# Kernel tuning notes

Hardware: AMD Instinct MI355X
Metric: run time of the kernel (lower is better)

Reference implementation:

```python
import jax, jax.numpy as jnp
import numpy as np

N = 50000        # nodes
E = 800000       # edges (avg degree 16)
D = 128          # input_dim
H = 128          # hidden_channels
OUT = 1          # output_dim
NUM_GRAPHS = 512 # graphs in batch (fixed for jit; == batch.max()+1)


def setup_inputs() -> dict:
    key = jax.random.key(0)
    ks = jax.random.split(key, 12)
    x = jax.random.normal(ks[0], (N, D), dtype=jnp.float32)
    edge_index = jax.random.randint(ks[1], (2, E), 0, N, dtype=jnp.int64)
    batch = jnp.sort(jax.random.randint(ks[2], (N,), 0, NUM_GRAPHS, dtype=jnp.int64))
    init = lambda k, shape, fan: jax.random.normal(k, shape, jnp.float32) * np.float32(1.0 / np.sqrt(fan))
    W1 = init(ks[3], (D, H), D); b1 = jnp.zeros((H,), jnp.float32)
    W2 = init(ks[4], (H, H), H); b2 = jnp.zeros((H,), jnp.float32)
    W3 = init(ks[5], (H, H), H); b3 = jnp.zeros((H,), jnp.float32)
    Wo = init(ks[6], (H, OUT), H); bo = jnp.zeros((OUT,), jnp.float32)
    return {"x": x, "edge_index": edge_index, "batch": batch,
            "W1": W1, "b1": b1, "W2": W2, "b2": b2, "W3": W3, "b3": b3,
            "Wo": Wo, "bo": bo}


def _gcn_layer(h, W, b, src, dst, dinv_sqrt):
    # GCNConv: x' = D^{-1/2}(A+I)D^{-1/2} X W + b  (self-loops added)
    hw = h @ W                                        # [N, H]
    coef = (dinv_sqrt[src] * dinv_sqrt[dst])[:, None] # [E, 1]
    agg = jax.ops.segment_sum(hw[src] * coef, dst, num_segments=N)
    agg = agg + hw * (dinv_sqrt * dinv_sqrt)[:, None] # self-loop term: deg^{-1}
    return agg + b


def reference(x, edge_index, batch, W1, b1, W2, b2, W3, b3, Wo, bo):
    src, dst = edge_index[0], edge_index[1]
    # degree from A+I (PyG computes deg on the target/col index)
    deg = jax.ops.segment_sum(jnp.ones((E,), x.dtype), dst, num_segments=N) + 1.0
    dinv_sqrt = jax.lax.rsqrt(deg)
    h = jax.nn.relu(_gcn_layer(x, W1, b1, src, dst, dinv_sqrt))
    h = jax.nn.relu(_gcn_layer(h, W2, b2, src, dst, dinv_sqrt))
    h = _gcn_layer(h, W3, b3, src, dst, dinv_sqrt)   # last conv: no relu
    pooled = jax.ops.segment_sum(h, batch, num_segments=NUM_GRAPHS)  # global_add_pool
    # F.dropout(p=0.1) is identity in eval mode
    return pooled @ Wo + bo                           # [NUM_GRAPHS, 1]
```

## Files before the change

### kernel.cpp

```cpp
#include <hip/hip_runtime.h>

typedef _Float16 f16;
typedef unsigned short u16;
typedef __attribute__((ext_vector_type(2))) _Float16 f16x2;
typedef __attribute__((ext_vector_type(8))) _Float16 f16x8;
typedef __attribute__((ext_vector_type(8))) unsigned short u16x8;
typedef __attribute__((ext_vector_type(4))) float f32x4;
typedef __attribute__((ext_vector_type(4))) int intx4;

#define STRIDE 64
#define SLAB   5120

__device__ inline float2 h2f(unsigned u){
    f16x2 h = __builtin_bit_cast(f16x2, u);
    return make_float2((float)h.x, (float)h.y);
}

__device__ inline void addrow(float* acc, uint4 u){
    float2 p0 = h2f(u.x), p1 = h2f(u.y), p2 = h2f(u.z), p3 = h2f(u.w);
    acc[0] += p0.x; acc[1] += p0.y; acc[2] += p1.x; acc[3] += p1.y;
    acc[4] += p2.x; acc[5] += p2.y; acc[6] += p3.x; acc[7] += p3.y;
}


__global__ __launch_bounds__(256) void k_bucket(const int* __restrict__ src, const int* __restrict__ dst,
                                                int* __restrict__ bucketCnt, unsigned* __restrict__ bucketBuf,
                                                int NB, int E4, int E){
    __shared__ int hist[256], pos[256];
    int t = threadIdx.x;
    hist[t] = 0;
    __syncthreads();
    int i4a = blockIdx.x*512 + t;
    int i4b = i4a + 256;
    bool va = i4a < E4, vb = i4b < E4;
    intx4 da = {}, db = {}, sa = {}, sb = {};
    if (va){ da = __builtin_nontemporal_load((const intx4*)dst + i4a);
             sa = __builtin_nontemporal_load((const intx4*)src + i4a); }
    if (vb){ db = __builtin_nontemporal_load((const intx4*)dst + i4b);
             sb = __builtin_nontemporal_load((const intx4*)src + i4b); }
    auto cnt1 = [&](int e, int d){ if (e < E) atomicAdd(&hist[d >> 8], 1); };
    if (va){ int b0 = i4a*4; cnt1(b0,da.x); cnt1(b0+1,da.y); cnt1(b0+2,da.z); cnt1(b0+3,da.w); }
    if (vb){ int b0 = i4b*4; cnt1(b0,db.x); cnt1(b0+1,db.y); cnt1(b0+2,db.z); cnt1(b0+3,db.w); }
    __syncthreads();
    if (t < NB && hist[t] > 0) pos[t] = atomicAdd(&bucketCnt[t], hist[t]);
    __syncthreads();
    auto put1 = [&](int e, int d, int s){
        if (e < E){
            int b = d >> 8;
            int slot = atomicAdd(&pos[b], 1);
            if (slot < SLAB)
                bucketBuf[(size_t)b*SLAB + slot] = ((unsigned)(d & 255) << 16) | (unsigned)s;
        }
    };
    if (va){ int b0 = i4a*4; put1(b0,da.x,sa.x); put1(b0+1,da.y,sa.y); put1(b0+2,da.z,sa.z); put1(b0+3,da.w,sa.w); }
    if (vb){ int b0 = i4b*4; put1(b0,db.x,sb.x); put1(b0+1,db.y,sb.y); put1(b0+2,db.z,sb.z); put1(b0+3,db.w,sb.w); }
}


__global__ __launch_bounds__(256) void k_build(const unsigned* __restrict__ bucketBuf,
                                               const int* __restrict__ bucketCnt,
                                               u16* __restrict__ csr, int* __restrict__ fil,
                                               float* __restrict__ dinv, int* __restrict__ blkh, int N){
    __shared__ u16 rows[256*64];
    __shared__ int cnt[256];
    __shared__ int h8[8];
    int t = threadIdx.x;
    cnt[t] = 0;
    if (t < 8) h8[t] = 0;
    u16x8 fillv;
    #pragma unroll
    for (int j = 0; j < 8; ++j) fillv[j] = (u16)N;
    #pragma unroll
    for (int j = 0; j < 8; ++j) *(u16x8*)&rows[t*64 + j*8] = fillv;
    __syncthreads();
    int b = blockIdx.x;
    int cb = min(bucketCnt[b], SLAB);
    for (int e = t; e < cb; e += 256){
        unsigned v = bucketBuf[(size_t)b*SLAB + e];
        int off = v >> 16;
        int p = atomicAdd(&cnt[off], 1);
        if (p < STRIDE){
            int ch = ((p >> 3) ^ (off & 7));
            rows[off*64 + ch*8 + (p & 7)] = (u16)(v & 0xffff);
        }
    }
    __syncthreads();
    int node = b*256 + t;
    if (node <= N){
        int c = cnt[t];
        fil[node] = c;
        dinv[node] = rsqrtf((float)c + 1.0f);
        if (node < N){
            int nb = (min(c, STRIDE) + 7) >> 3;
            if (nb > 7) nb = 7;
            atomicAdd(&h8[nb], 1);
        }
        u16x8* d8 = (u16x8*)&csr[(size_t)node*64];
        #pragma unroll
        for (int j = 0; j < 8; ++j)
            d8[j] = *(u16x8*)&rows[t*64 + ((j ^ (t & 7))*8)];
    }
    __syncthreads();
    if (t < 8) blkh[b*8 + t] = h8[t];
}

__global__ __launch_bounds__(256) void k_bscan(const int* __restrict__ blkh, int* __restrict__ blkoff,
                                               int* __restrict__ ord, uint4* __restrict__ hwrows,
                                               int N, int NQ4, int nbB){
    __shared__ int sm[8][256];
    int t = threadIdx.x;
    int v[8];
    #pragma unroll
    for (int b = 0; b < 8; ++b){
        v[b] = (t < nbB) ? blkh[t*8 + b] : 0;
        sm[b][t] = v[b];
    }
    __syncthreads();
    for (int off = 1; off < 256; off <<= 1){
        int u[8];
        #pragma unroll
        for (int b = 0; b < 8; ++b) u[b] = (t >= off) ? sm[b][t-off] : 0;
        __syncthreads();
        #pragma unroll
        for (int b = 0; b < 8; ++b) sm[b][t] += u[b];
        __syncthreads();
    }
    int s = 0;
    int bases[8];
    #pragma unroll
    for (int b = 0; b < 8; ++b){ bases[b] = s; s += sm[b][255]; }
    if (t < nbB){
        #pragma unroll
        for (int b = 0; b < 8; ++b)
            blkoff[t*8 + b] = sm[b][t] - v[b] + bases[b];
    }
    if (t >= 200 && t < 216) hwrows[(size_t)N*16 + (t - 200)] = make_uint4(0,0,0,0);
    for (int i = N + t; i < NQ4; i += 256) ord[i] = N;
}

__global__ __launch_bounds__(256) void k_scatterL(const int* __restrict__ fil, const int* __restrict__ blkoff,
                                                  int* __restrict__ ord, int N){
    __shared__ int off[8];
    int t = threadIdx.x;
    if (t < 8) off[t] = blkoff[blockIdx.x*8 + t];
    __syncthreads();
    int i = blockIdx.x*256 + t;
    if (i < N){
        int nb = (min(fil[i], STRIDE) + 7) >> 3;
        if (nb > 7) nb = 7;
        int p = atomicAdd(&off[nb], 1);
        ord[p] = i;
    }
}


__global__ __launch_bounds__(128) void k_prep(const float* __restrict__ W3, const float* __restrict__ Wo,
                                              const float* __restrict__ b3, float* __restrict__ u,
                                              float* __restrict__ su, float* __restrict__ zs,
                                              float* __restrict__ out, const float* __restrict__ bo,
                                              int N, int G){
    __shared__ float sWo[128];
    __shared__ float red[128];
    int t = threadIdx.x;
    sWo[t] = Wo[t];
    __syncthreads();
    float s = 0.f;
    for (int c2 = 0; c2 < 128; ++c2) s = fmaf(W3[t*128 + c2], sWo[c2], s);
    u[t] = s;
    red[t] = b3[t] * sWo[t];
    __syncthreads();
    for (int o = 64; o > 0; o >>= 1){
        if (t < o) red[t] += red[t+o];
        __syncthreads();
    }
    if (t == 0){ *su = red[0]; zs[N] = 0.f; }
    float bv = bo[0];
    for (int g2 = t; g2 < G; g2 += 128) out[g2] = bv;
}


#define LDW 136

template<int AFP16>
__global__ __launch_bounds__(256) void k_mm(const void* __restrict__ Av, const float* __restrict__ W,
                                            const float* __restrict__ dinv, f16* __restrict__ C, int n){
    __shared__ __align__(16) _Float16 sWt[128*LDW];
    __shared__ __align__(16) _Float16 sOut[4][16*LDW];
    int t = threadIdx.x;
    for (int idx = t; idx < 4096; idx += 256){
        int k = idx >> 5, c4 = (idx & 31) * 4;
        float4 w = ((const float4*)W)[idx];
        sWt[(c4+0)*LDW + k] = (f16)w.x;
        sWt[(c4+1)*LDW + k] = (f16)w.y;
        sWt[(c4+2)*LDW + k] = (f16)w.z;
        sWt[(c4+3)*LDW + k] = (f16)w.w;
    }
    __syncthreads();

    int wv = t >> 6, l = t & 63;
    int r16 = l & 15, g = l >> 4;
    int r0 = blockIdx.x * 64 + wv * 16;

    int arow = r0 + r16;
    bool aok = arow < n;
    f16x8 a[4];
    #pragma unroll
    for (int s = 0; s < 4; ++s){
        if (AFP16){
            const f16* A = (const f16*)Av;
            a[s] = aok ? *(const f16x8*)&A[(size_t)arow*128 + s*32 + g*8] : (f16x8)(_Float16)0.f;
        } else {
            const float* A = (const float*)Av;
            f16x8 av = (f16x8)(_Float16)0.f;
            if (aok){
                const float4* ap = (const float4*)&A[(size_t)arow*128 + s*32 + g*8];
                float4 x0 = ap[0], x1 = ap[1];
                av[0]=(f16)x0.x; av[1]=(f16)x0.y; av[2]=(f16)x0.z; av[3]=(f16)x0.w;
                av[4]=(f16)x1.x; av[5]=(f16)x1.y; av[6]=(f16)x1.z; av[7]=(f16)x1.w;
            }
            a[s] = av;
        }
    }

    f32x4 acc[8];
    #pragma unroll
    for (int ct = 0; ct < 8; ++ct) acc[ct] = (f32x4)0.f;

    #pragma unroll
    for (int ct = 0; ct < 8; ++ct){
        int c = ct*16 + r16;
        #pragma unroll
        for (int s = 0; s < 4; ++s){
            f16x8 b = *(const f16x8*)&sWt[c*LDW + s*32 + g*8];
            acc[ct] = __builtin_amdgcn_mfma_f32_16x16x32_f16(a[s], b, acc[ct], 0, 0, 0);
        }
    }

    float dv[4];
    #pragma unroll
    for (int j = 0; j < 4; ++j){
        int rr = r0 + g*4 + j;
        dv[j] = (rr < n) ? dinv[rr] : 0.f;
    }
    #pragma unroll
    for (int ct = 0; ct < 8; ++ct)
        #pragma unroll
        for (int j = 0; j < 4; ++j)
            sOut[wv][(g*4+j)*LDW + ct*16 + r16] = (f16)(acc[ct][j] * dv[j]);
    __syncthreads();

    int orow = r0 + r16;
    if (orow < n){
        const f16x8* srcp = (const f16x8*)&sOut[wv][r16*LDW + g*32];
        f16x8 o0 = srcp[0], o1 = srcp[1], o2 = srcp[2], o3 = srcp[3];
        f16x8* dstp = (f16x8*)&C[(size_t)orow*128 + g*32];
        dstp[0]=o0; dstp[1]=o1; dstp[2]=o2; dstp[3]=o3;
    }
}


#define AGG_BODY \
    int l = threadIdx.x & 63; \
    int g = l >> 4, c = l & 15; \
    intx4 wq = *((const intx4*)ord + wvi); \
    int w0 = __builtin_amdgcn_readfirstlane(wq.x); \
    int w1 = __builtin_amdgcn_readfirstlane(wq.y); \
    int w2 = __builtin_amdgcn_readfirstlane(wq.z); \
    int w3 = __builtin_amdgcn_readfirstlane(wq.w); \
    int wsel = (g==0) ? w0 : (g==1) ? w1 : (g==2) ? w2 : w3; \
    const uint4* rows = (const uint4*)hw; \
    float acc[8] = {0,0,0,0,0,0,0,0}; \
    { uint4 s = rows[(size_t)wsel*16 + c]; addrow(acc, s); } \
    int nb0=(min(fil[w0],STRIDE)+7)>>3, nb1=(min(fil[w1],STRIDE)+7)>>3; \
    int nb2=(min(fil[w2],STRIDE)+7)>>3, nb3=(min(fil[w3],STRIDE)+7)>>3; \
    int nbm  = max(max(nb0,nb1), max(nb2,nb3)); \
    int nbsel = (g==0) ? nb0 : (g==1) ? nb1 : (g==2) ? nb2 : nb3; \
    const u16* cp = csr + (size_t)wsel*STRIDE; \
    for (int t2 = 0; t2 < nbm; ++t2){ \
        if (t2 < nbsel){ \
            u16x8 iv = *(const u16x8*)cp; cp += 8; \
            uint4 r0 = rows[(size_t)iv[0]*16 + c]; \
            uint4 r1 = rows[(size_t)iv[1]*16 + c]; \
            uint4 r2 = rows[(size_t)iv[2]*16 + c]; \
            uint4 r3 = rows[(size_t)iv[3]*16 + c]; \
            uint4 r4 = rows[(size_t)iv[4]*16 + c]; \
            uint4 r5 = rows[(size_t)iv[5]*16 + c]; \
            uint4 r6 = rows[(size_t)iv[6]*16 + c]; \
            uint4 r7 = rows[(size_t)iv[7]*16 + c]; \
            addrow(acc, r0); addrow(acc, r1); addrow(acc, r2); addrow(acc, r3); \
            addrow(acc, r4); addrow(acc, r5); addrow(acc, r6); addrow(acc, r7); \
        } \
    }

__global__ __launch_bounds__(256) void k_agg4(const f16* __restrict__ hw, const float* __restrict__ dinv,
                                              const int* __restrict__ fil, const u16* __restrict__ csr,
                                              const int* __restrict__ ord, const float* __restrict__ bias,
                                              f16* __restrict__ hout, int N, int NQ){
    int wvi = (blockIdx.x*256 + threadIdx.x) >> 6;
    if (wvi >= NQ) return;
    AGG_BODY
    if (wsel < N){
        float di = dinv[wsel];
        const float4* bp = (const float4*)bias + c*2;
        float4 b0 = bp[0], b1 = bp[1];
        f16x8 o;
        o[0]=(f16)fmaxf(fmaf(acc[0],di,b0.x),0.f); o[1]=(f16)fmaxf(fmaf(acc[1],di,b0.y),0.f);
        o[2]=(f16)fmaxf(fmaf(acc[2],di,b0.z),0.f); o[3]=(f16)fmaxf(fmaf(acc[3],di,b0.w),0.f);
        o[4]=(f16)fmaxf(fmaf(acc[4],di,b1.x),0.f); o[5]=(f16)fmaxf(fmaf(acc[5],di,b1.y),0.f);
        o[6]=(f16)fmaxf(fmaf(acc[6],di,b1.z),0.f); o[7]=(f16)fmaxf(fmaf(acc[7],di,b1.w),0.f);
        *(f16x8*)&hout[(size_t)wsel*128 + c*8] = o;
    }
}

__global__ __launch_bounds__(256) void k_agg4z(const f16* __restrict__ hw, const float* __restrict__ dinv,
                                               const int* __restrict__ fil, const u16* __restrict__ csr,
                                               const int* __restrict__ ord, const float* __restrict__ bias,
                                               const float* __restrict__ u, float* __restrict__ zs,
                                               int N, int NQ){
    int wvi = (blockIdx.x*256 + threadIdx.x) >> 6;
    if (wvi >= NQ) return;
    AGG_BODY
    float di = dinv[wsel];
    const float4* bp = (const float4*)bias + c*2;
    const float4* up = (const float4*)u    + c*2;
    float4 b0 = bp[0], b1 = bp[1];
    float4 u0 = up[0], u1 = up[1];
    float dot = fmaxf(fmaf(acc[0],di,b0.x),0.f)*u0.x + fmaxf(fmaf(acc[1],di,b0.y),0.f)*u0.y
              + fmaxf(fmaf(acc[2],di,b0.z),0.f)*u0.z + fmaxf(fmaf(acc[3],di,b0.w),0.f)*u0.w
              + fmaxf(fmaf(acc[4],di,b1.x),0.f)*u1.x + fmaxf(fmaf(acc[5],di,b1.y),0.f)*u1.y
              + fmaxf(fmaf(acc[6],di,b1.z),0.f)*u1.z + fmaxf(fmaf(acc[7],di,b1.w),0.f)*u1.w;
    dot += __shfl_xor(dot, 1);
    dot += __shfl_xor(dot, 2);
    dot += __shfl_xor(dot, 4);
    dot += __shfl_xor(dot, 8);
    if (c == 0 && wsel < N) zs[wsel] = di * dot;
}


__global__ __launch_bounds__(256) void k_aggs(const float* __restrict__ zs, const float* __restrict__ dinv,
                                              const int* __restrict__ fil, const u16* __restrict__ csr,
                                              const int* __restrict__ batch, const float* __restrict__ supt,
                                              float* __restrict__ out, int N){
    __shared__ float bins[512];
    int t = threadIdx.x;
    bins[t] = 0.f; bins[t+256] = 0.f;
    __syncthreads();
    int i = blockIdx.x*256 + t;
    if (i < N){
        float acc = zs[i];
        int nb = (min(fil[i], STRIDE) + 7) >> 3;
        const u16* cp = csr + (size_t)i*STRIDE;
        for (int b = 0; b < nb; ++b){
            u16x8 iv = *(const u16x8*)cp; cp += 8;
            float s0 = zs[iv[0]] + zs[iv[1]], s1 = zs[iv[2]] + zs[iv[3]];
            float s2 = zs[iv[4]] + zs[iv[5]], s3 = zs[iv[6]] + zs[iv[7]];
            acc += (s0 + s1) + (s2 + s3);
        }
        float tv = fmaf(dinv[i], acc, *supt);
        atomicAdd(&bins[batch[i]], tv);
    }
    __syncthreads();
    float v0 = bins[t], v1 = bins[t+256];
    if (v0 != 0.f) atomicAdd(&out[t], v0);
    if (v1 != 0.f) atomicAdd(&out[t+256], v1);
}


extern "C" void kernel_launch(void* const* d_in, const int* in_sizes, int n_in,
                              void* d_out, int out_size, void* d_ws, size_t ws_size,
                              hipStream_t stream) {
    const float* x     = (const float*)d_in[0];
    const int*   ei    = (const int*)d_in[1];
    const int*   batch = (const int*)d_in[2];
    const float* W1 = (const float*)d_in[3];
    const float* b1 = (const float*)d_in[4];
    const float* W2 = (const float*)d_in[5];
    const float* b2 = (const float*)d_in[6];
    const float* W3 = (const float*)d_in[7];
    const float* b3 = (const float*)d_in[8];
    const float* Wo = (const float*)d_in[9];
    const float* bo = (const float*)d_in[10];

    int N = in_sizes[0] / 128;
    int E = in_sizes[1] / 2;
    int G = out_size;
    const int* srcI = ei;
    const int* dstI = ei + E;

    int NQ  = (N + 3) / 4;
    int NQ4 = NQ * 4;
    int NB  = (N + 256) / 256;
    int E4  = (E + 3) / 4;
    int nbK = (E + 2047) / 2048;

    char* p = (char*)d_ws;
    size_t off = 0;
    auto alloc = [&](size_t bytes) -> void* {
        void* r = p + off;
        off += (bytes + 255) & ~(size_t)255;
        return r;
    };
    f16*      hw      = (f16*)alloc((size_t)(N+1)*128*sizeof(f16));
    f16*      h       = (f16*)alloc((size_t)N*128*sizeof(f16));
    float*    dinv    = (float*)alloc((size_t)(N+1)*sizeof(float));
    int*      fil     = (int*)alloc((size_t)(N+1)*sizeof(int));
    int*      blkh    = (int*)alloc((size_t)NB*8*sizeof(int));
    int*      blkoff  = (int*)alloc((size_t)NB*8*sizeof(int));
    int*      ord     = (int*)alloc((size_t)NQ4*sizeof(int));
    float*    zs      = (float*)alloc((size_t)(N+1)*sizeof(float));
    float*    uvec    = (float*)alloc(128*sizeof(float));
    float*    su      = (float*)alloc(sizeof(float));
    int*      bucketCnt = (int*)alloc((size_t)NB*sizeof(int));
    unsigned* bucketBuf = (unsigned*)alloc((size_t)NB*SLAB*sizeof(unsigned));
    u16*      csr     = (u16*)alloc((size_t)(N+1)*STRIDE*sizeof(u16));

    hipMemsetAsync(bucketCnt, 0, (size_t)NB*sizeof(int), stream);

    k_bucket  <<<nbK, 256, 0, stream>>>(srcI, dstI, bucketCnt, bucketBuf, NB, E4, E);
    k_build   <<<NB,  256, 0, stream>>>(bucketBuf, bucketCnt, csr, fil, dinv, blkh, N);
    k_bscan   <<<1,   256, 0, stream>>>(blkh, blkoff, ord, (uint4*)hw, N, NQ4, NB);
    k_scatterL<<<NB,  256, 0, stream>>>(fil, blkoff, ord, N);
    k_prep    <<<1,   128, 0, stream>>>(W3, Wo, b3, uvec, su, zs, (float*)d_out, bo, N, G);

    int nbM = (N + 63)/64;
    int nbA = (int)(((size_t)NQ*64 + 255)/256);

    k_mm<0> <<<nbM, 256, 0, stream>>>(x, W1, dinv, hw, N);
    k_agg4  <<<nbA, 256, 0, stream>>>(hw, dinv, fil, csr, ord, b1, h, N, NQ);
    k_mm<1> <<<nbM, 256, 0, stream>>>(h, W2, dinv, hw, N);
    k_agg4z <<<nbA, 256, 0, stream>>>(hw, dinv, fil, csr, ord, b2, uvec, zs, N, NQ);
    k_aggs  <<<NB,  256, 0, stream>>>(zs, dinv, fil, csr, batch, su, (float*)d_out, N);
}
```

Before: 161.6 us.

## Fuse all GCN pipeline stages into one cooperative persistent kernel with grid syncs

Replaces the chain of ten kernel launches plus a memset with a single cooperative persistent kernel. Each former kernel becomes a grid-stride phase separated by grid.sync(), and a shared-memory union is reused across phases. The aim is to remove launch gaps and the tails of the small single-block kernels. In exchange it pays for grid-wide barriers, the matmul phase now serialises its four waves' output staging through one smaller sOut buffer, and host occupancy queries run on every call. The old multi-kernel path stays as a fallback.

```diff
diff --git a/kernel.cpp b/kernel.cpp
--- a/kernel.cpp
+++ b/kernel.cpp
@@ -1,4 +1,7 @@
 #include <hip/hip_runtime.h>
+#include <hip/hip_cooperative_groups.h>
+
+namespace cg = cooperative_groups;
 
 typedef _Float16 f16;
 typedef unsigned short u16;
@@ -10,6 +13,7 @@
 
 #define STRIDE 64
 #define SLAB   5120
+#define LDW    136
 
 __device__ inline float2 h2f(unsigned u){
     f16x2 h = __builtin_bit_cast(f16x2, u);
@@ -21,243 +25,6 @@
     acc[0] += p0.x; acc[1] += p0.y; acc[2] += p1.x; acc[3] += p1.y;
     acc[4] += p2.x; acc[5] += p2.y; acc[6] += p3.x; acc[7] += p3.y;
 }
-
-
-__global__ __launch_bounds__(256) void k_bucket(const int* __restrict__ src, const int* __restrict__ dst,
-                                                int* __restrict__ bucketCnt, unsigned* __restrict__ bucketBuf,
-                                                int NB, int E4, int E){
-    __shared__ int hist[256], pos[256];
-    int t = threadIdx.x;
-    hist[t] = 0;
-    __syncthreads();
-    int i4a = blockIdx.x*512 + t;
-    int i4b = i4a + 256;
-    bool va = i4a < E4, vb = i4b < E4;
-    intx4 da = {}, db = {}, sa = {}, sb = {};
-    if (va){ da = __builtin_nontemporal_load((const intx4*)dst + i4a);
-             sa = __builtin_nontemporal_load((const intx4*)src + i4a); }
-    if (vb){ db = __builtin_nontemporal_load((const intx4*)dst + i4b);
-             sb = __builtin_nontemporal_load((const intx4*)src + i4b); }
-    auto cnt1 = [&](int e, int d){ if (e < E) atomicAdd(&hist[d >> 8], 1); };
-    if (va){ int b0 = i4a*4; cnt1(b0,da.x); cnt1(b0+1,da.y); cnt1(b0+2,da.z); cnt1(b0+3,da.w); }
-    if (vb){ int b0 = i4b*4; cnt1(b0,db.x); cnt1(b0+1,db.y); cnt1(b0+2,db.z); cnt1(b0+3,db.w); }
-    __syncthreads();
-    if (t < NB && hist[t] > 0) pos[t] = atomicAdd(&bucketCnt[t], hist[t]);
-    __syncthreads();
-    auto put1 = [&](int e, int d, int s){
-        if (e < E){
-            int b = d >> 8;
-            int slot = atomicAdd(&pos[b], 1);
-            if (slot < SLAB)
-                bucketBuf[(size_t)b*SLAB + slot] = ((unsigned)(d & 255) << 16) | (unsigned)s;
-        }
-    };
-    if (va){ int b0 = i4a*4; put1(b0,da.x,sa.x); put1(b0+1,da.y,sa.y); put1(b0+2,da.z,sa.z); put1(b0+3,da.w,sa.w); }
-    if (vb){ int b0 = i4b*4; put1(b0,db.x,sb.x); put1(b0+1,db.y,sb.y); put1(b0+2,db.z,sb.z); put1(b0+3,db.w,sb.w); }
-}
-
-
-__global__ __launch_bounds__(256) void k_build(const unsigned* __restrict__ bucketBuf,
-                                               const int* __restrict__ bucketCnt,
-                                               u16* __restrict__ csr, int* __restrict__ fil,
-                                               float* __restrict__ dinv, int* __restrict__ blkh, int N){
-    __shared__ u16 rows[256*64];
-    __shared__ int cnt[256];
-    __shared__ int h8[8];
-    int t = threadIdx.x;
-    cnt[t] = 0;
-    if (t < 8) h8[t] = 0;
-    u16x8 fillv;
-    #pragma unroll
-    for (int j = 0; j < 8; ++j) fillv[j] = (u16)N;
-    #pragma unroll
-    for (int j = 0; j < 8; ++j) *(u16x8*)&rows[t*64 + j*8] = fillv;
-    __syncthreads();
-    int b = blockIdx.x;
-    int cb = min(bucketCnt[b], SLAB);
-    for (int e = t; e < cb; e += 256){
-        unsigned v = bucketBuf[(size_t)b*SLAB + e];
-        int off = v >> 16;
-        int p = atomicAdd(&cnt[off], 1);
-        if (p < STRIDE){
-            int ch = ((p >> 3) ^ (off & 7));
-            rows[off*64 + ch*8 + (p & 7)] = (u16)(v & 0xffff);
-        }
-    }
-    __syncthreads();
-    int node = b*256 + t;
-    if (node <= N){
-        int c = cnt[t];
-        fil[node] = c;
-        dinv[node] = rsqrtf((float)c + 1.0f);
-        if (node < N){
-            int nb = (min(c, STRIDE) + 7) >> 3;
-            if (nb > 7) nb = 7;
-            atomicAdd(&h8[nb], 1);
-        }
-        u16x8* d8 = (u16x8*)&csr[(size_t)node*64];
-        #pragma unroll
-        for (int j = 0; j < 8; ++j)
-            d8[j] = *(u16x8*)&rows[t*64 + ((j ^ (t & 7))*8)];
-    }
-    __syncthreads();
-    if (t < 8) blkh[b*8 + t] = h8[t];
-}
-
-__global__ __launch_bounds__(256) void k_bscan(const int* __restrict__ blkh, int* __restrict__ blkoff,
-                                               int* __restrict__ ord, uint4* __restrict__ hwrows,
-                                               int N, int NQ4, int nbB){
-    __shared__ int sm[8][256];
-    int t = threadIdx.x;
-    int v[8];
-    #pragma unroll
-    for (int b = 0; b < 8; ++b){
-        v[b] = (t < nbB) ? blkh[t*8 + b] : 0;
-        sm[b][t] = v[b];
-    }
-    __syncthreads();
-    for (int off = 1; off < 256; off <<= 1){
-        int u[8];
-        #pragma unroll
-        for (int b = 0; b < 8; ++b) u[b] = (t >= off) ? sm[b][t-off] : 0;
-        __syncthreads();
-        #pragma unroll
-        for (int b = 0; b < 8; ++b) sm[b][t] += u[b];
-        __syncthreads();
-    }
-    int s = 0;
-    int bases[8];
-    #pragma unroll
-    for (int b = 0; b < 8; ++b){ bases[b] = s; s += sm[b][255]; }
-    if (t < nbB){
-        #pragma unroll
-        for (int b = 0; b < 8; ++b)
-            blkoff[t*8 + b] = sm[b][t] - v[b] + bases[b];
-    }
-    if (t >= 200 && t < 216) hwrows[(size_t)N*16 + (t - 200)] = make_uint4(0,0,0,0);
-    for (int i = N + t; i < NQ4; i += 256) ord[i] = N;
-}
-
-__global__ __launch_bounds__(256) void k_scatterL(const int* __restrict__ fil, const int* __restrict__ blkoff,
-                                                  int* __restrict__ ord, int N){
-    __shared__ int off[8];
-    int t = threadIdx.x;
-    if (t < 8) off[t] = blkoff[blockIdx.x*8 + t];
-    __syncthreads();
-    int i = blockIdx.x*256 + t;
-    if (i < N){
-        int nb = (min(fil[i], STRIDE) + 7) >> 3;
-        if (nb > 7) nb = 7;
-        int p = atomicAdd(&off[nb], 1);
-        ord[p] = i;
-    }
-}
-
-
-__global__ __launch_bounds__(128) void k_prep(const float* __restrict__ W3, const float* __restrict__ Wo,
-                                              const float* __restrict__ b3, float* __restrict__ u,
-                                              float* __restrict__ su, float* __restrict__ zs,
-                                              float* __restrict__ out, const float* __restrict__ bo,
-                                              int N, int G){
-    __shared__ float sWo[128];
-    __shared__ float red[128];
-    int t = threadIdx.x;
-    sWo[t] = Wo[t];
-    __syncthreads();
-    float s = 0.f;
-    for (int c2 = 0; c2 < 128; ++c2) s = fmaf(W3[t*128 + c2], sWo[c2], s);
-    u[t] = s;
-    red[t] = b3[t] * sWo[t];
-    __syncthreads();
-    for (int o = 64; o > 0; o >>= 1){
-        if (t < o) red[t] += red[t+o];
-        __syncthreads();
-    }
-    if (t == 0){ *su = red[0]; zs[N] = 0.f; }
-    float bv = bo[0];
-    for (int g2 = t; g2 < G; g2 += 128) out[g2] = bv;
-}
-
-
-#define LDW 136
-
-template<int AFP16>
-__global__ __launch_bounds__(256) void k_mm(const void* __restrict__ Av, const float* __restrict__ W,
-                                            const float* __restrict__ dinv, f16* __restrict__ C, int n){
-    __shared__ __align__(16) _Float16 sWt[128*LDW];
-    __shared__ __align__(16) _Float16 sOut[4][16*LDW];
-    int t = threadIdx.x;
-    for (int idx = t; idx < 4096; idx += 256){
-        int k = idx >> 5, c4 = (idx & 31) * 4;
-        float4 w = ((const float4*)W)[idx];
-        sWt[(c4+0)*LDW + k] = (f16)w.x;
-        sWt[(c4+1)*LDW + k] = (f16)w.y;
-        sWt[(c4+2)*LDW + k] = (f16)w.z;
-        sWt[(c4+3)*LDW + k] = (f16)w.w;
-    }
-    __syncthreads();
-
-    int wv = t >> 6, l = t & 63;
-    int r16 = l & 15, g = l >> 4;
-    int r0 = blockIdx.x * 64 + wv * 16;
-
-    int arow = r0 + r16;
-    bool aok = arow < n;
-    f16x8 a[4];
-    #pragma unroll
-    for (int s = 0; s < 4; ++s){
-        if (AFP16){
-            const f16* A = (const f16*)Av;
-            a[s] = aok ? *(const f16x8*)&A[(size_t)arow*128 + s*32 + g*8] : (f16x8)(_Float16)0.f;
-        } else {
-            const float* A = (const float*)Av;
-            f16x8 av = (f16x8)(_Float16)0.f;
-            if (aok){
-                const float4* ap = (const float4*)&A[(size_t)arow*128 + s*32 + g*8];
-                float4 x0 = ap[0], x1 = ap[1];
-                av[0]=(f16)x0.x; av[1]=(f16)x0.y; av[2]=(f16)x0.z; av[3]=(f16)x0.w;
-                av[4]=(f16)x1.x; av[5]=(f16)x1.y; av[6]=(f16)x1.z; av[7]=(f16)x1.w;
-            }
-            a[s] = av;
-        }
-    }
-
-    f32x4 acc[8];
-    #pragma unroll
-    for (int ct = 0; ct < 8; ++ct) acc[ct] = (f32x4)0.f;
-
-    #pragma unroll
-    for (int ct = 0; ct < 8; ++ct){
-        int c = ct*16 + r16;
-        #pragma unroll
-        for (int s = 0; s < 4; ++s){
-            f16x8 b = *(const f16x8*)&sWt[c*LDW + s*32 + g*8];
-            acc[ct] = __builtin_amdgcn_mfma_f32_16x16x32_f16(a[s], b, acc[ct], 0, 0, 0);
-        }
-    }
-
-    float dv[4];
-    #pragma unroll
-    for (int j = 0; j < 4; ++j){
-        int rr = r0 + g*4 + j;
-        dv[j] = (rr < n) ? dinv[rr] : 0.f;
-    }
-    #pragma unroll
-    for (int ct = 0; ct < 8; ++ct)
-        #pragma unroll
-        for (int j = 0; j < 4; ++j)
-            sOut[wv][(g*4+j)*LDW + ct*16 + r16] = (f16)(acc[ct][j] * dv[j]);
-    __syncthreads();
-
-    int orow = r0 + r16;
-    if (orow < n){
-        const f16x8* srcp = (const f16x8*)&sOut[wv][r16*LDW + g*32];
-        f16x8 o0 = srcp[0], o1 = srcp[1], o2 = srcp[2], o3 = srcp[3];
-        f16x8* dstp = (f16x8*)&C[(size_t)orow*128 + g*32];
-        dstp[0]=o0; dstp[1]=o1; dstp[2]=o2; dstp[3]=o3;
-    }
-}
-
 
 #define AGG_BODY \
     int l = threadIdx.x & 63; \
@@ -292,6 +59,496 @@
         } \
     }
 
+
+template<int AFP16>
+__device__ __forceinline__ void mm_body(const void* Av, const float* W, const float* dinv,
+                                        f16* C, int n, int vb, _Float16* sWt, _Float16* sOut){
+    int t = threadIdx.x;
+    for (int idx = t; idx < 4096; idx += 256){
+        int k = idx >> 5, c4 = (idx & 31) * 4;
+        float4 w = ((const float4*)W)[idx];
+        sWt[(c4+0)*LDW + k] = (f16)w.x;
+        sWt[(c4+1)*LDW + k] = (f16)w.y;
+        sWt[(c4+2)*LDW + k] = (f16)w.z;
+        sWt[(c4+3)*LDW + k] = (f16)w.w;
+    }
+    __syncthreads();
+
+    int wv = t >> 6, l = t & 63;
+    int r16 = l & 15, g = l >> 4;
+    int r0 = vb * 64 + wv * 16;
+
+    int arow = r0 + r16;
+    bool aok = arow < n;
+    f16x8 a[4];
+    #pragma unroll
+    for (int s = 0; s < 4; ++s){
+        if (AFP16){
+            const f16* A = (const f16*)Av;
+            a[s] = aok ? *(const f16x8*)&A[(size_t)arow*128 + s*32 + g*8] : (f16x8)(_Float16)0.f;
+        } else {
+            const float* A = (const float*)Av;
+            f16x8 av = (f16x8)(_Float16)0.f;
+            if (aok){
+                const float4* ap = (const float4*)&A[(size_t)arow*128 + s*32 + g*8];
+                float4 x0 = ap[0], x1 = ap[1];
+                av[0]=(f16)x0.x; av[1]=(f16)x0.y; av[2]=(f16)x0.z; av[3]=(f16)x0.w;
+                av[4]=(f16)x1.x; av[5]=(f16)x1.y; av[6]=(f16)x1.z; av[7]=(f16)x1.w;
+            }
+            a[s] = av;
+        }
+    }
+
+    f32x4 acc[8];
+    #pragma unroll
+    for (int ct = 0; ct < 8; ++ct) acc[ct] = (f32x4)0.f;
+    #pragma unroll
+    for (int ct = 0; ct < 8; ++ct){
+        int c = ct*16 + r16;
+        #pragma unroll
+        for (int s = 0; s < 4; ++s){
+            f16x8 b = *(const f16x8*)&sWt[c*LDW + s*32 + g*8];
+            acc[ct] = __builtin_amdgcn_mfma_f32_16x16x32_f16(a[s], b, acc[ct], 0, 0, 0);
+        }
+    }
+
+    float dv[4];
+    #pragma unroll
+    for (int j = 0; j < 4; ++j){
+        int rr = r0 + g*4 + j;
+        dv[j] = (rr < n) ? dinv[rr] : 0.f;
+    }
+    for (int s4 = 0; s4 < 4; ++s4){
+        if (wv == s4){
+            #pragma unroll
+            for (int ct = 0; ct < 8; ++ct)
+                #pragma unroll
+                for (int j = 0; j < 4; ++j)
+                    sOut[(g*4+j)*LDW + ct*16 + r16] = (f16)(acc[ct][j] * dv[j]);
+        }
+        __syncthreads();
+        if (wv == s4){
+            int orow = r0 + r16;
+            if (orow < n){
+                const f16x8* sp = (const f16x8*)&sOut[r16*LDW + g*32];
+                f16x8 o0 = sp[0], o1 = sp[1], o2 = sp[2], o3 = sp[3];
+                f16x8* dp = (f16x8*)&C[(size_t)orow*128 + g*32];
+                dp[0]=o0; dp[1]=o1; dp[2]=o2; dp[3]=o3;
+            }
+        }
+        __syncthreads();
+    }
+}
+
+
+struct Params {
+    const float* x; const int* srcI; const int* dstI; const int* batch;
+    const float* W1; const float* b1; const float* W2; const float* b2;
+    const float* W3; const float* b3; const float* Wo; const float* bo;
+    float* out;
+    f16* hw; f16* h; float* dinv; int* fil; int* blkh; int* blkoff;
+    int* ord; float* zs; float* uvec; float* su; int* bucketCnt; unsigned* bucketBuf;
+    u16* csr;
+    int N, E, E4, G, NB, NQ, NQ4, nbK, nbM;
+};
+
+__global__ __launch_bounds__(256, 4) void k_mega(Params P){
+    cg::grid_group grid = cg::this_grid();
+    int t = threadIdx.x;
+    int nP = gridDim.x;
+
+    __shared__ __align__(16) union {
+        struct { int hist[256]; int pos[256]; } bk;
+        struct { u16 rows[256*64]; int cnt[256]; int h8[8]; } bd;
+        struct { int sm[8][256]; } sc;
+        struct { _Float16 sWt[128*LDW]; _Float16 sOut[16*LDW]; } mm;
+        struct { float bins[512]; } ag;
+        struct { float sWo[128]; float red[128]; } pr;
+        struct { int off[8]; } st;
+    } S;
+
+    if (blockIdx.x == 0){
+        if (t < 128) S.pr.sWo[t] = P.Wo[t];
+        __syncthreads();
+        if (t < 128){
+            float s = 0.f;
+            for (int k = 0; k < 128; ++k) s = fmaf(P.W3[t*128 + k], S.pr.sWo[k], s);
+            P.uvec[t] = s;
+            S.pr.red[t] = P.b3[t] * S.pr.sWo[t];
+        }
+        __syncthreads();
+        for (int o = 64; o > 0; o >>= 1){
+            if (t < o && t < 128) S.pr.red[t] += S.pr.red[t+o];
+            __syncthreads();
+        }
+        if (t == 0){ *P.su = S.pr.red[0]; P.zs[P.N] = 0.f; }
+        float bv = P.bo[0];
+        for (int g2 = t; g2 < P.G; g2 += 256) P.out[g2] = bv;
+    } else {
+        for (int i = (blockIdx.x-1)*256 + t; i < P.NB; i += (nP-1)*256) P.bucketCnt[i] = 0;
+    }
+    grid.sync();
+
+    for (int vb = blockIdx.x; vb < P.nbK; vb += nP){
+        S.bk.hist[t] = 0;
+        __syncthreads();
+        int i4a = vb*512 + t, i4b = i4a + 256;
+        bool va = i4a < P.E4, vvb = i4b < P.E4;
+        intx4 da = {}, db = {}, sa = {}, sb = {};
+        if (va){ da = __builtin_nontemporal_load((const intx4*)P.dstI + i4a);
+                 sa = __builtin_nontemporal_load((const intx4*)P.srcI + i4a); }
+        if (vvb){ db = __builtin_nontemporal_load((const intx4*)P.dstI + i4b);
+                  sb = __builtin_nontemporal_load((const intx4*)P.srcI + i4b); }
+        auto cnt1 = [&](int e, int d){ if (e < P.E) atomicAdd(&S.bk.hist[d >> 8], 1); };
+        if (va){ int b0 = i4a*4; cnt1(b0,da.x); cnt1(b0+1,da.y); cnt1(b0+2,da.z); cnt1(b0+3,da.w); }
+        if (vvb){ int b0 = i4b*4; cnt1(b0,db.x); cnt1(b0+1,db.y); cnt1(b0+2,db.z); cnt1(b0+3,db.w); }
+        __syncthreads();
+        if (t < P.NB && S.bk.hist[t] > 0) S.bk.pos[t] = atomicAdd(&P.bucketCnt[t], S.bk.hist[t]);
+        __syncthreads();
+        auto put1 = [&](int e, int d, int s){
+            if (e < P.E){
+                int b = d >> 8;
+                int slot = atomicAdd(&S.bk.pos[b], 1);
+                if (slot < SLAB)
+                    P.bucketBuf[(size_t)b*SLAB + slot] = ((unsigned)(d & 255) << 16) | (unsigned)s;
+            }
+        };
+        if (va){ int b0 = i4a*4; put1(b0,da.x,sa.x); put1(b0+1,da.y,sa.y); put1(b0+2,da.z,sa.z); put1(b0+3,da.w,sa.w); }
+        if (vvb){ int b0 = i4b*4; put1(b0,db.x,sb.x); put1(b0+1,db.y,sb.y); put1(b0+2,db.z,sb.z); put1(b0+3,db.w,sb.w); }
+        __syncthreads();
+    }
+    grid.sync();
+
+    for (int vb = blockIdx.x; vb < P.NB; vb += nP){
+        S.bd.cnt[t] = 0;
+        if (t < 8) S.bd.h8[t] = 0;
+        u16x8 fillv;
+        #pragma unroll
+        for (int j = 0; j < 8; ++j) fillv[j] = (u16)P.N;
+        #pragma unroll
+        for (int j = 0; j < 8; ++j) *(u16x8*)&S.bd.rows[t*64 + j*8] = fillv;
+        __syncthreads();
+        int cb = min(P.bucketCnt[vb], SLAB);
+        for (int e = t; e < cb; e += 256){
+            unsigned v = P.bucketBuf[(size_t)vb*SLAB + e];
+            int off = v >> 16;
+            int slot = atomicAdd(&S.bd.cnt[off], 1);
+            if (slot < STRIDE){
+                int ch = ((slot >> 3) ^ (off & 7));
+                S.bd.rows[off*64 + ch*8 + (slot & 7)] = (u16)(v & 0xffff);
+            }
+        }
+        __syncthreads();
+        int node = vb*256 + t;
+        if (node <= P.N){
+            int c = S.bd.cnt[t];
+            P.fil[node] = c;
+            P.dinv[node] = rsqrtf((float)c + 1.0f);
+            if (node < P.N){
+                int nb = (min(c, STRIDE) + 7) >> 3;
+                if (nb > 7) nb = 7;
+                atomicAdd(&S.bd.h8[nb], 1);
+            }
+            u16x8* d8 = (u16x8*)&P.csr[(size_t)node*64];
+            #pragma unroll
+            for (int j = 0; j < 8; ++j)
+                d8[j] = *(u16x8*)&S.bd.rows[t*64 + ((j ^ (t & 7))*8)];
+        }
+        __syncthreads();
+        if (t < 8) P.blkh[vb*8 + t] = S.bd.h8[t];
+        __syncthreads();
+    }
+    grid.sync();
+
+    if (blockIdx.x == 0){
+        int v[8];
+        #pragma unroll
+        for (int b = 0; b < 8; ++b){
+            v[b] = (t < P.NB) ? P.blkh[t*8 + b] : 0;
+            S.sc.sm[b][t] = v[b];
+        }
+        __syncthreads();
+        for (int off = 1; off < 256; off <<= 1){
+            int u[8];
+            #pragma unroll
+            for (int b = 0; b < 8; ++b) u[b] = (t >= off) ? S.sc.sm[b][t-off] : 0;
+            __syncthreads();
+            #pragma unroll
+            for (int b = 0; b < 8; ++b) S.sc.sm[b][t] += u[b];
+            __syncthreads();
+        }
+        int s = 0;
+        int bases[8];
+        #pragma unroll
+        for (int b = 0; b < 8; ++b){ bases[b] = s; s += S.sc.sm[b][255]; }
+        if (t < P.NB){
+            #pragma unroll
+            for (int b = 0; b < 8; ++b)
+                P.blkoff[t*8 + b] = S.sc.sm[b][t] - v[b] + bases[b];
+        }
+    }
+    if (blockIdx.x == 1){
+        if (t < 16) ((uint4*)P.hw)[(size_t)P.N*16 + t] = make_uint4(0,0,0,0);
+        for (int i = P.N + t; i < P.NQ4; i += 256) P.ord[i] = P.N;
+    }
+    grid.sync();
+
+    for (int vb = blockIdx.x; vb < P.NB + P.nbM; vb += nP){
+        if (vb < P.NB){
+            if (t < 8) S.st.off[t] = P.blkoff[vb*8 + t];
+            __syncthreads();
+            int i = vb*256 + t;
+            if (i < P.N){
+                int nb = (min(P.fil[i], STRIDE) + 7) >> 3;
+                if (nb > 7) nb = 7;
+                int pos = atomicAdd(&S.st.off[nb], 1);
+                P.ord[pos] = i;
+            }
+            __syncthreads();
+        } else {
+            mm_body<0>(P.x, P.W1, P.dinv, P.hw, P.N, vb - P.NB, S.mm.sWt, S.mm.sOut);
+        }
+    }
+    grid.sync();
+
+    {
+        const f16* hw = P.hw; const int* fil = P.fil; const u16* csr = P.csr;
+        const int* ord = P.ord; int N = P.N;
+        int waveId = blockIdx.x*4 + (t >> 6);
+        int nW = nP*4;
+        for (int wvi = waveId; wvi < P.NQ; wvi += nW){
+            AGG_BODY
+            if (wsel < N){
+                float di = P.dinv[wsel];
+                const float4* bp = (const float4*)P.b1 + c*2;
+                float4 b0 = bp[0], b1v = bp[1];
+                f16x8 o;
+                o[0]=(f16)fmaxf(fmaf(acc[0],di,b0.x),0.f); o[1]=(f16)fmaxf(fmaf(acc[1],di,b0.y),0.f);
+                o[2]=(f16)fmaxf(fmaf(acc[2],di,b0.z),0.f); o[3]=(f16)fmaxf(fmaf(acc[3],di,b0.w),0.f);
+                o[4]=(f16)fmaxf(fmaf(acc[4],di,b1v.x),0.f); o[5]=(f16)fmaxf(fmaf(acc[5],di,b1v.y),0.f);
+                o[6]=(f16)fmaxf(fmaf(acc[6],di,b1v.z),0.f); o[7]=(f16)fmaxf(fmaf(acc[7],di,b1v.w),0.f);
+                *(f16x8*)&P.h[(size_t)wsel*128 + c*8] = o;
+            }
+        }
+    }
+    grid.sync();
+
+    for (int vb = blockIdx.x; vb < P.nbM; vb += nP)
+        mm_body<1>(P.h, P.W2, P.dinv, P.hw, P.N, vb, S.mm.sWt, S.mm.sOut);
+    grid.sync();
+
+    {
+        const f16* hw = P.hw; const int* fil = P.fil; const u16* csr = P.csr;
+        const int* ord = P.ord; int N = P.N;
+        int waveId = blockIdx.x*4 + (t >> 6);
+        int nW = nP*4;
+        for (int wvi = waveId; wvi < P.NQ; wvi += nW){
+            AGG_BODY
+            float di = P.dinv[wsel];
+            const float4* bp = (const float4*)P.b2 + c*2;
+            const float4* up = (const float4*)P.uvec + c*2;
+            float4 b0 = bp[0], b1v = bp[1];
+            float4 u0 = up[0], u1 = up[1];
+            float dot = fmaxf(fmaf(acc[0],di,b0.x),0.f)*u0.x + fmaxf(fmaf(acc[1],di,b0.y),0.f)*u0.y
+                      + fmaxf(fmaf(acc[2],di,b0.z),0.f)*u0.z + fmaxf(fmaf(acc[3],di,b0.w),0.f)*u0.w
+                      + fmaxf(fmaf(acc[4],di,b1v.x),0.f)*u1.x + fmaxf(fmaf(acc[5],di,b1v.y),0.f)*u1.y
+                      + fmaxf(fmaf(acc[6],di,b1v.z),0.f)*u1.z + fmaxf(fmaf(acc[7],di,b1v.w),0.f)*u1.w;
+            dot += __shfl_xor(dot, 1);
+            dot += __shfl_xor(dot, 2);
+            dot += __shfl_xor(dot, 4);
+            dot += __shfl_xor(dot, 8);
+            if (c == 0 && wsel < N) P.zs[wsel] = di * dot;
+        }
+    }
+    grid.sync();
+
+    for (int vb = blockIdx.x; vb < P.NB; vb += nP){
+        S.ag.bins[t] = 0.f; S.ag.bins[t+256] = 0.f;
+        __syncthreads();
+        int i = vb*256 + t;
+        if (i < P.N){
+            float acc = P.zs[i];
+            int nb = (min(P.fil[i], STRIDE) + 7) >> 3;
+            const u16* cp = P.csr + (size_t)i*STRIDE;
+            for (int b = 0; b < nb; ++b){
+                u16x8 iv = *(const u16x8*)cp; cp += 8;
+                float s0 = P.zs[iv[0]] + P.zs[iv[1]], s1 = P.zs[iv[2]] + P.zs[iv[3]];
+                float s2 = P.zs[iv[4]] + P.zs[iv[5]], s3 = P.zs[iv[6]] + P.zs[iv[7]];
+                acc += (s0 + s1) + (s2 + s3);
+            }
+            float tv = fmaf(P.dinv[i], acc, *P.su);
+            atomicAdd(&S.ag.bins[P.batch[i]], tv);
+        }
+        __syncthreads();
+        float v0 = S.ag.bins[t], v1 = S.ag.bins[t+256];
+        if (v0 != 0.f) atomicAdd(&P.out[t], v0);
+        if (v1 != 0.f) atomicAdd(&P.out[t+256], v1);
+        __syncthreads();
+    }
+}
+
+
+__global__ __launch_bounds__(256) void k_bucket(const int* __restrict__ src, const int* __restrict__ dst,
+                                                int* __restrict__ bucketCnt, unsigned* __restrict__ bucketBuf,
+                                                int NB, int E4, int E){
+    __shared__ int hist[256], pos[256];
+    int t = threadIdx.x;
+    hist[t] = 0;
+    __syncthreads();
+    int i4a = blockIdx.x*512 + t;
+    int i4b = i4a + 256;
+    bool va = i4a < E4, vb = i4b < E4;
+    intx4 da = {}, db = {}, sa = {}, sb = {};
+    if (va){ da = __builtin_nontemporal_load((const intx4*)dst + i4a);
+             sa = __builtin_nontemporal_load((const intx4*)src + i4a); }
+    if (vb){ db = __builtin_nontemporal_load((const intx4*)dst + i4b);
+             sb = __builtin_nontemporal_load((const intx4*)src + i4b); }
+    auto cnt1 = [&](int e, int d){ if (e < E) atomicAdd(&hist[d >> 8], 1); };
+    if (va){ int b0 = i4a*4; cnt1(b0,da.x); cnt1(b0+1,da.y); cnt1(b0+2,da.z); cnt1(b0+3,da.w); }
+    if (vb){ int b0 = i4b*4; cnt1(b0,db.x); cnt1(b0+1,db.y); cnt1(b0+2,db.z); cnt1(b0+3,db.w); }
+    __syncthreads();
+    if (t < NB && hist[t] > 0) pos[t] = atomicAdd(&bucketCnt[t], hist[t]);
+    __syncthreads();
+    auto put1 = [&](int e, int d, int s){
+        if (e < E){
+            int b = d >> 8;
+            int slot = atomicAdd(&pos[b], 1);
+            if (slot < SLAB)
+                bucketBuf[(size_t)b*SLAB + slot] = ((unsigned)(d & 255) << 16) | (unsigned)s;
+        }
+    };
+    if (va){ int b0 = i4a*4; put1(b0,da.x,sa.x); put1(b0+1,da.y,sa.y); put1(b0+2,da.z,sa.z); put1(b0+3,da.w,sa.w); }
+    if (vb){ int b0 = i4b*4; put1(b0,db.x,sb.x); put1(b0+1,db.y,sb.y); put1(b0+2,db.z,sb.z); put1(b0+3,db.w,sb.w); }
+}
+
+__global__ __launch_bounds__(256) void k_build(const unsigned* __restrict__ bucketBuf,
+                                               const int* __restrict__ bucketCnt,
+                                               u16* __restrict__ csr, int* __restrict__ fil,
+                                               float* __restrict__ dinv, int* __restrict__ blkh, int N){
+    __shared__ u16 rows[256*64];
+    __shared__ int cnt[256];
+    __shared__ int h8[8];
+    int t = threadIdx.x;
+    cnt[t] = 0;
+    if (t < 8) h8[t] = 0;
+    u16x8 fillv;
+    #pragma unroll
+    for (int j = 0; j < 8; ++j) fillv[j] = (u16)N;
+    #pragma unroll
+    for (int j = 0; j < 8; ++j) *(u16x8*)&rows[t*64 + j*8] = fillv;
+    __syncthreads();
+    int b = blockIdx.x;
+    int cb = min(bucketCnt[b], SLAB);
+    for (int e = t; e < cb; e += 256){
+        unsigned v = bucketBuf[(size_t)b*SLAB + e];
+        int off = v >> 16;
+        int p = atomicAdd(&cnt[off], 1);
+        if (p < STRIDE){
+            int ch = ((p >> 3) ^ (off & 7));
+            rows[off*64 + ch*8 + (p & 7)] = (u16)(v & 0xffff);
+        }
+    }
+    __syncthreads();
+    int node = b*256 + t;
+    if (node <= N){
+        int c = cnt[t];
+        fil[node] = c;
+        dinv[node] = rsqrtf((float)c + 1.0f);
+        if (node < N){
+            int nb = (min(c, STRIDE) + 7) >> 3;
+            if (nb > 7) nb = 7;
+            atomicAdd(&h8[nb], 1);
+        }
+        u16x8* d8 = (u16x8*)&csr[(size_t)node*64];
+        #pragma unroll
+        for (int j = 0; j < 8; ++j)
+            d8[j] = *(u16x8*)&rows[t*64 + ((j ^ (t & 7))*8)];
+    }
+    __syncthreads();
+    if (t < 8) blkh[b*8 + t] = h8[t];
+}
+
+__global__ __launch_bounds__(256) void k_bscan(const int* __restrict__ blkh, int* __restrict__ blkoff,
+                                               int* __restrict__ ord, uint4* __restrict__ hwrows,
+                                               int N, int NQ4, int nbB){
+    __shared__ int sm[8][256];
+    int t = threadIdx.x;
+    int v[8];
+    #pragma unroll
+    for (int b = 0; b < 8; ++b){
+        v[b] = (t < nbB) ? blkh[t*8 + b] : 0;
+        sm[b][t] = v[b];
+    }
+    __syncthreads();
+    for (int off = 1; off < 256; off <<= 1){
+        int u[8];
+        #pragma unroll
+        for (int b = 0; b < 8; ++b) u[b] = (t >= off) ? sm[b][t-off] : 0;
+        __syncthreads();
+        #pragma unroll
+        for (int b = 0; b < 8; ++b) sm[b][t] += u[b];
+        __syncthreads();
+    }
+    int s = 0;
+    int bases[8];
+    #pragma unroll
+    for (int b = 0; b < 8; ++b){ bases[b] = s; s += sm[b][255]; }
+    if (t < nbB){
+        #pragma unroll
+        for (int b = 0; b < 8; ++b)
+            blkoff[t*8 + b] = sm[b][t] - v[b] + bases[b];
+    }
+    if (t >= 200 && t < 216) hwrows[(size_t)N*16 + (t - 200)] = make_uint4(0,0,0,0);
+    for (int i = N + t; i < NQ4; i += 256) ord[i] = N;
+}
+
+__global__ __launch_bounds__(256) void k_scatterL(const int* __restrict__ fil, const int* __restrict__ blkoff,
+                                                  int* __restrict__ ord, int N){
+    __shared__ int off[8];
+    int t = threadIdx.x;
+    if (t < 8) off[t] = blkoff[blockIdx.x*8 + t];
+    __syncthreads();
+    int i = blockIdx.x*256 + t;
+    if (i < N){
+        int nb = (min(fil[i], STRIDE) + 7) >> 3;
+        if (nb > 7) nb = 7;
+        int p = atomicAdd(&off[nb], 1);
+        ord[p] = i;
+    }
+}
+
+__global__ __launch_bounds__(128) void k_prep(const float* __restrict__ W3, const float* __restrict__ Wo,
+                                              const float* __restrict__ b3, float* __restrict__ u,
+                                              float* __restrict__ su, float* __restrict__ zs,
+                                              float* __restrict__ out, const float* __restrict__ bo,
+                                              int N, int G){
+    __shared__ float sWo[128];
+    __shared__ float red[128];
+    int t = threadIdx.x;
+    sWo[t] = Wo[t];
+    __syncthreads();
+    float s = 0.f;
+    for (int c2 = 0; c2 < 128; ++c2) s = fmaf(W3[t*128 + c2], sWo[c2], s);
+    u[t] = s;
+    red[t] = b3[t] * sWo[t];
+    __syncthreads();
+    for (int o = 64; o > 0; o >>= 1){
+        if (t < o) red[t] += red[t+o];
+        __syncthreads();
+    }
+    if (t == 0){ *su = red[0]; zs[N] = 0.f; }
+    float bv = bo[0];
+    for (int g2 = t; g2 < G; g2 += 128) out[g2] = bv;
+}
+
+template<int AFP16>
+__global__ __launch_bounds__(256) void k_mm(const void* __restrict__ Av, const float* __restrict__ W,
+                                            const float* __restrict__ dinv, f16* __restrict__ C, int n){
+    __shared__ __align__(16) _Float16 sWt[128*LDW];
+    __shared__ __align__(16) _Float16 sOut[16*LDW];
+    mm_body<AFP16>(Av, W, dinv, C, n, blockIdx.x, sWt, sOut);
+}
+
 __global__ __launch_bounds__(256) void k_agg4(const f16* __restrict__ hw, const float* __restrict__ dinv,
                                               const int* __restrict__ fil, const u16* __restrict__ csr,
                                               const int* __restrict__ ord, const float* __restrict__ bias,
@@ -336,7 +593,6 @@
     if (c == 0 && wsel < N) zs[wsel] = di * dot;
 }
 
-
 __global__ __launch_bounds__(256) void k_aggs(const float* __restrict__ zs, const float* __restrict__ dinv,
                                               const int* __restrict__ fil, const u16* __restrict__ csr,
                                               const int* __restrict__ batch, const float* __restrict__ supt,
@@ -392,6 +648,7 @@
     int NB  = (N + 256) / 256;
     int E4  = (E + 3) / 4;
     int nbK = (E + 2047) / 2048;
+    int nbM = (N + 63) / 64;
 
     char* p = (char*)d_ws;
     size_t off = 0;
@@ -409,25 +666,50 @@
     int*      ord     = (int*)alloc((size_t)NQ4*sizeof(int));
     float*    zs      = (float*)alloc((size_t)(N+1)*sizeof(float));
     float*    uvec    = (float*)alloc(128*sizeof(float));
-    float*    su      = (float*)alloc(sizeof(float));
+    float*    su      = (float*)alloc(256);
     int*      bucketCnt = (int*)alloc((size_t)NB*sizeof(int));
     unsigned* bucketBuf = (unsigned*)alloc((size_t)NB*SLAB*sizeof(unsigned));
     u16*      csr     = (u16*)alloc((size_t)(N+1)*STRIDE*sizeof(u16));
 
-    hipMemsetAsync(bucketCnt, 0, (size_t)NB*sizeof(int), stream);
-
-    k_bucket  <<<nbK, 256, 0, stream>>>(srcI, dstI, bucketCnt, bucketBuf, NB, E4, E);
-    k_build   <<<NB,  256, 0, stream>>>(bucketBuf, bucketCnt, csr, fil, dinv, blkh, N);
-    k_bscan   <<<1,   256, 0, stream>>>(blkh, blkoff, ord, (uint4*)hw, N, NQ4, NB);
-    k_scatterL<<<NB,  256, 0, stream>>>(fil, blkoff, ord, N);
-    k_prep    <<<1,   128, 0, stream>>>(W3, Wo, b3, uvec, su, zs, (float*)d_out, bo, N, G);
-
-    int nbM = (N + 63)/64;
-    int nbA = (int)(((size_t)NQ*64 + 255)/256);
-
-    k_mm<0> <<<nbM, 256, 0, stream>>>(x, W1, dinv, hw, N);
-    k_agg4  <<<nbA, 256, 0, stream>>>(hw, dinv, fil, csr, ord, b1, h, N, NQ);
-    k_mm<1> <<<nbM, 256, 0, stream>>>(h, W2, dinv, hw, N);
-    k_agg4z <<<nbA, 256, 0, stream>>>(hw, dinv, fil, csr, ord, b2, uvec, zs, N, NQ);
-    k_aggs  <<<NB,  256, 0, stream>>>(zs, dinv, fil, csr, batch, su, (float*)d_out, N);
-}
+    int coop = 0, dev = 0, nCU = 0, blkPerCU = 0;
+    hipGetDevice(&dev);
+    hipDeviceGetAttribute(&coop, hipDeviceAttributeCooperativeLaunch, dev);
+    hipDeviceGetAttribute(&nCU, hipDeviceAttributeMultiprocessorCount, dev);
+    hipError_t occ = hipOccupancyMaxActiveBlocksPerMultiprocessor(&blkPerCU, k_mega, 256, 0);
+
+    bool done = false;
+    if (coop && occ == hipSuccess && blkPerCU > 0 && nCU > 0){
+        Params prm;
+        prm.x = x; prm.srcI = srcI; prm.dstI = dstI; prm.batch = batch;
+        prm.W1 = W1; prm.b1 = b1; prm.W2 = W2; prm.b2 = b2;
+        prm.W3 = W3; prm.b3 = b3; prm.Wo = Wo; prm.bo = bo;
+        prm.out = (float*)d_out;
+        prm.hw = hw; prm.h = h; prm.dinv = dinv; prm.fil = fil;
+        prm.blkh = blkh; prm.blkoff = blkoff; prm.ord = ord; prm.zs = zs;
+        prm.uvec = uvec; prm.su = su; prm.bucketCnt = bucketCnt; prm.bucketBuf = bucketBuf;
+        prm.csr = csr;
+        prm.N = N; prm.E = E; prm.E4 = E4; prm.G = G; prm.NB = NB;
+        prm.NQ = NQ; prm.NQ4 = NQ4; prm.nbK = nbK; prm.nbM = nbM;
+
+        int grid = blkPerCU * nCU;
+        if (grid > 2048) grid = 2048;
+        void* args[] = { (void*)&prm };
+        hipError_t err = hipLaunchCooperativeKernel(k_mega, dim3(grid), dim3(256), args, 0u, stream);
+        if (err == hipSuccess) done = true;
+    }
+
+    if (!done){
+        hipMemsetAsync(bucketCnt, 0, (size_t)NB*sizeof(int), stream);
+        k_bucket  <<<nbK, 256, 0, stream>>>(srcI, dstI, bucketCnt, bucketBuf, NB, E4, E);
+        k_build   <<<NB,  256, 0, stream>>>(bucketBuf, bucketCnt, csr, fil, dinv, blkh, N);
+        k_bscan   <<<1,   256, 0, stream>>>(blkh, blkoff, ord, (uint4*)hw, N, NQ4, NB);
+        k_scatterL<<<NB,  256, 0, stream>>>(fil, blkoff, ord, N);
+        k_prep    <<<1,   128, 0, stream>>>(W3, Wo, b3, uvec, su, zs, (float*)d_out, bo, N, G);
+        int nbA = (int)(((size_t)NQ*64 + 255)/256);
+        k_mm<0> <<<nbM, 256, 0, stream>>>(x, W1, dinv, hw, N);
+        k_agg4  <<<nbA, 256, 0, stream>>>(hw, dinv, fil, csr, ord, b1, h, N, NQ);
+        k_mm<1> <<<nbM, 256, 0, stream>>>(h, W2, dinv, hw, N);
+        k_agg4z <<<nbA, 256, 0, stream>>>(hw, dinv, fil, csr, ord, b2, uvec, zs, N, NQ);
+        k_aggs  <<<NB,  256, 0, stream>>>(zs, dinv, fil, csr, batch, su, (float*)d_out, N);
+    }
+}
```

New measurement: 636.5 us. 3.94x slower.
